# Kernel tuning notes

Measured on AMD Instinct MI355X. Metric: run time of the kernel, lower is better.

Reference implementation:

```python
import jax, jax.numpy as jnp
import numpy as np

N_NODES = 100000
N_EDGES = 1600000
NEG_SLOPE = 0.2  # PyG GATConv default


def _gat_layer(x, src, dst, W, a_src, a_dst, b, heads, concat):
    """One PyG-style GATConv (eval mode, self-loops already appended)."""
    N = x.shape[0]
    xp = (x @ W).reshape(N, heads, -1)                      # [N, H, C]
    al_s = jnp.einsum('nhc,hc->nh', xp, a_src)              # [N, H]
    al_d = jnp.einsum('nhc,hc->nh', xp, a_dst)              # [N, H]
    e = jax.nn.leaky_relu(al_s[src] + al_d[dst], NEG_SLOPE)  # [E, H]
    # numerically stable segment softmax over incoming edges of each dst
    m = jax.ops.segment_max(e, dst, num_segments=N)         # [N, H]
    ex = jnp.exp(e - m[dst])
    s = jax.ops.segment_sum(ex, dst, num_segments=N)
    alpha = ex / (s[dst] + 1e-16)                           # [E, H]
    out = jax.ops.segment_sum(xp[src] * alpha[:, :, None], dst, num_segments=N)  # [N, H, C]
    out = out.reshape(N, -1) if concat else out.mean(axis=1)
    return out + b


def setup_inputs() -> dict:
    key = jax.random.key(0)
    ks = jax.random.split(key, 16)
    H, C0 = 4, 32  # hidden layers: 4 heads x 32 = 128
    inp = {
        'x': jax.random.normal(ks[0], (N_NODES, 128), dtype=jnp.float32),
        'edge_index': jax.random.randint(ks[1], (2, N_EDGES), 0, N_NODES, dtype=jnp.int64),
        'W0': jax.random.normal(ks[2], (128, 128), dtype=jnp.float32) * 0.1,
        'a_src0': jax.random.normal(ks[3], (H, C0), dtype=jnp.float32) * 0.1,
        'a_dst0': jax.random.normal(ks[4], (H, C0), dtype=jnp.float32) * 0.1,
        'b0': jnp.zeros((128,), dtype=jnp.float32),
        'W1': jax.random.normal(ks[5], (128, 128), dtype=jnp.float32) * 0.1,
        'a_src1': jax.random.normal(ks[6], (H, C0), dtype=jnp.float32) * 0.1,
        'a_dst1': jax.random.normal(ks[7], (H, C0), dtype=jnp.float32) * 0.1,
        'b1': jnp.zeros((128,), dtype=jnp.float32),
        'W2': jax.random.normal(ks[8], (128, 64), dtype=jnp.float32) * 0.1,
        'a_src2': jax.random.normal(ks[9], (1, 64), dtype=jnp.float32) * 0.1,
        'a_dst2': jax.random.normal(ks[10], (1, 64), dtype=jnp.float32) * 0.1,
        'b2': jnp.zeros((64,), dtype=jnp.float32),
    }
    return inp


def reference(x, edge_index, W0, a_src0, a_dst0, b0, W1, a_src1, a_dst1, b1, W2, a_src2, a_dst2, b2):
    N = x.shape[0]
    loop = jnp.arange(N, dtype=edge_index.dtype)
    src = jnp.concatenate([edge_index[0], loop])  # add_self_loops=True
    dst = jnp.concatenate([edge_index[1], loop])
    h = _gat_layer(x, src, dst, W0, a_src0, a_dst0, b0, heads=4, concat=True)
    h = jax.nn.elu(h)
    h = _gat_layer(h, src, dst, W1, a_src1, a_dst1, b1, heads=4, concat=True)
    h = jax.nn.elu(h)
    out = _gat_layer(h, src, dst, W2, a_src2, a_dst2, b2, heads=1, concat=False)
    return out
```

## Files before the change

### kernel.cpp

```cpp
#include <hip/hip_runtime.h>
#include <math.h>


#define N_NODES 100000
#define NBUCK ((N_NODES + 255) / 256)

typedef __attribute__((ext_vector_type(4))) _Float16 half4;
typedef __attribute__((ext_vector_type(8))) _Float16 half8;
typedef __attribute__((ext_vector_type(4))) float f32x4;


__global__ __launch_bounds__(256) void k_bcount(const int* __restrict__ ei, int E, int ETOT,
                                                int* __restrict__ bucketCnt) {
    __shared__ int h[NBUCK];
    for (int b = threadIdx.x; b < NBUCK; b += 256) h[b] = 0;
    __syncthreads();
    const int base = blockIdx.x * 4096;
#pragma unroll
    for (int j = 0; j < 16; ++j) {
        int idx = base + j * 256 + threadIdx.x;
        if (idx < ETOT) {
            int dst = (idx < E) ? ei[E + idx] : (idx - E);
            atomicAdd(&h[dst >> 8], 1);
        }
    }
    __syncthreads();
    for (int b = threadIdx.x; b < NBUCK; b += 256)
        if (h[b]) atomicAdd(&bucketCnt[b], h[b]);
}

__global__ __launch_bounds__(256) void k_bscan(const int* __restrict__ bucketCnt,
                                               int* __restrict__ bstart,
                                               int* __restrict__ gcur, int ETOT) {
    __shared__ int lds[512];
    const int t = threadIdx.x;
    lds[t] = (t < NBUCK) ? bucketCnt[t] : 0;
    lds[t + 256] = (t + 256 < NBUCK) ? bucketCnt[t + 256] : 0;
    __syncthreads();
    for (int d = 1; d < 512; d <<= 1) {
        int v0 = (t >= d) ? lds[t - d] : 0;
        int v1 = (t + 256 >= d) ? lds[t + 256 - d] : 0;
        __syncthreads();
        lds[t] += v0;
        lds[t + 256] += v1;
        __syncthreads();
    }
    int e0 = (t == 0) ? 0 : lds[t - 1];
    int e1 = lds[t + 255];
    if (t < NBUCK)       { bstart[t] = e0;       gcur[t] = e0; }
    if (t + 256 < NBUCK) { bstart[t + 256] = e1; gcur[t + 256] = e1; }
    if (t == 0) bstart[NBUCK] = ETOT;
}

__global__ __launch_bounds__(256) void k_bplace(const int* __restrict__ ei, int E, int ETOT,
                                                int* __restrict__ gcur, int* __restrict__ tmp) {
    __shared__ int h[NBUCK];
    __shared__ int cur[NBUCK];
    for (int b = threadIdx.x; b < NBUCK; b += 256) h[b] = 0;
    __syncthreads();
    const int base = blockIdx.x * 4096;
    int pk[16], bk[16];
#pragma unroll
    for (int j = 0; j < 16; ++j) {
        int idx = base + j * 256 + threadIdx.x;
        bk[j] = -1;
        if (idx < ETOT) {
            int s, d;
            if (idx < E) { s = ei[idx]; d = ei[E + idx]; }
            else         { s = idx - E; d = idx - E; }
            bk[j] = d >> 8;
            pk[j] = s | ((d & 255) << 17);
            atomicAdd(&h[bk[j]], 1);
        }
    }
    __syncthreads();
    for (int b = threadIdx.x; b < NBUCK; b += 256)
        cur[b] = h[b] ? atomicAdd(&gcur[b], h[b]) : 0;
    __syncthreads();
#pragma unroll
    for (int j = 0; j < 16; ++j) {
        if (bk[j] >= 0) {
            int pos = atomicAdd(&cur[bk[j]], 1);
            tmp[pos] = pk[j];
        }
    }
}

__global__ __launch_bounds__(256) void k_bfinal(const int* __restrict__ tmp,
                                                const int* __restrict__ bstart,
                                                int* __restrict__ rowptr,
                                                int* __restrict__ ssrc, int N) {
    __shared__ int cnt[256];
    __shared__ int cur[256];
    const int t = threadIdx.x;
    const int b = blockIdx.x;
    const int s0 = bstart[b], s1 = bstart[b + 1];
    cnt[t] = 0;
    __syncthreads();
    for (int e = s0 + t; e < s1; e += 256)
        atomicAdd(&cnt[tmp[e] >> 17], 1);
    __syncthreads();
    int c0 = cnt[t];
    for (int d = 1; d < 256; d <<= 1) {
        int v = (t >= d) ? cnt[t - d] : 0;
        __syncthreads();
        cnt[t] += v;
        __syncthreads();
    }
    int excl = cnt[t] - c0;
    int node = b * 256 + t;
    if (node <= N) rowptr[node] = s0 + excl;
    cur[t] = excl;
    __syncthreads();
    for (int e = s0 + t; e < s1; e += 256) {
        int p = tmp[e];
        int pos = atomicAdd(&cur[p >> 17], 1);
        ssrc[s0 + pos] = p & 0x1FFFF;
    }
}

__global__ void k_wt(const float* __restrict__ W, _Float16* __restrict__ Wt, int OUTn) {
    int idx = blockIdx.x * 256 + threadIdx.x;
    if (idx >= 128 * OUTn) return;
    int k = idx / OUTn, n = idx % OUTn;
    Wt[n * 128 + k] = (_Float16)W[idx];
}

template <int OUT, int H>
__global__ __launch_bounds__(256) void k_gemm(const float* __restrict__ X,
                                              const _Float16* __restrict__ Wt,
                                              const float* __restrict__ a_src,
                                              const float* __restrict__ a_dst,
                                              _Float16* __restrict__ XP,
                                              float* __restrict__ al_s,
                                              float* __restrict__ al_d, int N) {
    constexpr int NT = OUT / 16;
    constexpr int C = OUT / H;
    constexpr int LDH = 136;
    __shared__ _Float16 As[64 * LDH];
    __shared__ _Float16 Ws[OUT * LDH];
    const int tid = threadIdx.x;
    const int row0 = blockIdx.x * 64;

    for (int c = tid; c < OUT * 16; c += 256) {
        int r = c >> 4, kc = c & 15;
        *(half8*)&Ws[r * LDH + kc * 8] = *(const half8*)(Wt + r * 128 + kc * 8);
    }
    for (int c = tid; c < 64 * 16; c += 256) {
        int r = c >> 4, kc = c & 15;
        int grow = row0 + r;
        half8 hv;
        if (grow < N) {
            const float4* xr = (const float4*)(X + (size_t)grow * 128 + kc * 8);
            float4 x0 = xr[0], x1 = xr[1];
            hv[0] = (_Float16)x0.x; hv[1] = (_Float16)x0.y;
            hv[2] = (_Float16)x0.z; hv[3] = (_Float16)x0.w;
            hv[4] = (_Float16)x1.x; hv[5] = (_Float16)x1.y;
            hv[6] = (_Float16)x1.z; hv[7] = (_Float16)x1.w;
        } else {
#pragma unroll
            for (int j = 0; j < 8; ++j) hv[j] = (_Float16)0.f;
        }
        *(half8*)&As[r * LDH + kc * 8] = hv;
    }
    __syncthreads();

    const int w = tid >> 6;
    const int l = tid & 63;
    const int lm = l & 15;
    const int lk = l >> 4;

    f32x4 acc[NT];
#pragma unroll
    for (int nt = 0; nt < NT; ++nt) acc[nt] = {0.f, 0.f, 0.f, 0.f};

#pragma unroll
    for (int ks = 0; ks < 4; ++ks) {
        half8 av = *(const half8*)&As[(w * 16 + lm) * LDH + ks * 32 + lk * 8];
#pragma unroll
        for (int nt = 0; nt < NT; ++nt) {
            half8 bv = *(const half8*)&Ws[(nt * 16 + lm) * LDH + ks * 32 + lk * 8];
            acc[nt] = __builtin_amdgcn_mfma_f32_16x16x32_f16(av, bv, acc[nt], 0, 0, 0);
        }
    }

    float avs[NT], avd[NT];
#pragma unroll
    for (int nt = 0; nt < NT; ++nt) {
        avs[nt] = a_src[nt * 16 + lm];
        avd[nt] = a_dst[nt * 16 + lm];
    }

#pragma unroll
    for (int r = 0; r < 4; ++r) {
        int grow = row0 + w * 16 + lk * 4 + r;
        bool ok = grow < N;
#pragma unroll
        for (int nt = 0; nt < NT; ++nt)
            if (ok) XP[(size_t)grow * OUT + nt * 16 + lm] = (_Float16)acc[nt][r];

        float ps[H], pd[H];
#pragma unroll
        for (int h = 0; h < H; ++h) { ps[h] = 0.f; pd[h] = 0.f; }
#pragma unroll
        for (int nt = 0; nt < NT; ++nt) {
            int h = (nt * 16) / C;
            ps[h] += acc[nt][r] * avs[nt];
            pd[h] += acc[nt][r] * avd[nt];
        }
#pragma unroll
        for (int h = 0; h < H; ++h) {
#pragma unroll
            for (int o = 8; o >= 1; o >>= 1) {
                ps[h] += __shfl_xor(ps[h], o);
                pd[h] += __shfl_xor(pd[h], o);
            }
        }
        if (ok && lm == 0) {
#pragma unroll
            for (int h = 0; h < H; ++h) {
                al_s[(size_t)grow * H + h] = ps[h];
                al_d[(size_t)grow * H + h] = pd[h];
            }
        }
    }
}

template <int OUT, int H, bool ELU>
__global__ __launch_bounds__(256) void k_agg(const _Float16* __restrict__ xp,
                                             const float* __restrict__ al_s,
                                             const float* __restrict__ al_d,
                                             const int* __restrict__ rowptr,
                                             const int* __restrict__ ssrc,
                                             const float* __restrict__ bias,
                                             float* __restrict__ out, int N) {
    constexpr int C = OUT / H;
    constexpr int CPL = OUT / 16;
    const int wid = threadIdx.x >> 6;
    const int lane = threadIdx.x & 63;
    const int qid = lane >> 4;
    const int l4 = lane & 15;
    const int node = blockIdx.x * 4 + wid;
    if (node >= N) return;
    const int rs = rowptr[node];
    const int re = rowptr[node + 1];

    const int c0 = l4 * CPL;
    const int hd = c0 / C;
    const float adh = al_d[(size_t)node * H + hd];

    float ssum = 0.f;
    float acc[CPL];
#pragma unroll
    for (int j = 0; j < CPL; ++j) acc[j] = 0.f;

    int i = rs;
    for (; i + 8 <= re; i += 8) {
        int sA = ssrc[i + qid];
        int sB = ssrc[i + qid + 4];
        float eA = al_s[(size_t)sA * H + hd] + adh; eA = eA > 0.f ? eA : 0.2f * eA;
        float eB = al_s[(size_t)sB * H + hd] + adh; eB = eB > 0.f ? eB : 0.2f * eB;
        float aA = __expf(eA);
        float aB = __expf(eB);
        ssum += aA + aB;
        if constexpr (CPL == 8) {
            half8 vA = *(const half8*)(xp + (size_t)sA * OUT + c0);
            half8 vB = *(const half8*)(xp + (size_t)sB * OUT + c0);
#pragma unroll
            for (int j = 0; j < 8; ++j) acc[j] += aA * (float)vA[j] + aB * (float)vB[j];
        } else {
            half4 vA = *(const half4*)(xp + (size_t)sA * OUT + c0);
            half4 vB = *(const half4*)(xp + (size_t)sB * OUT + c0);
#pragma unroll
            for (int j = 0; j < 4; ++j) acc[j] += aA * (float)vA[j] + aB * (float)vB[j];
        }
    }
    for (; i + qid < re; i += 4) {
        int s = ssrc[i + qid];
        float e = al_s[(size_t)s * H + hd] + adh; e = e > 0.f ? e : 0.2f * e;
        float a = __expf(e);
        ssum += a;
        if constexpr (CPL == 8) {
            half8 v = *(const half8*)(xp + (size_t)s * OUT + c0);
#pragma unroll
            for (int j = 0; j < 8; ++j) acc[j] += a * (float)v[j];
        } else {
            half4 v = *(const half4*)(xp + (size_t)s * OUT + c0);
#pragma unroll
            for (int j = 0; j < 4; ++j) acc[j] += a * (float)v[j];
        }
    }

    ssum += __shfl_xor(ssum, 16);
    ssum += __shfl_xor(ssum, 32);
#pragma unroll
    for (int j = 0; j < CPL; ++j) {
        acc[j] += __shfl_xor(acc[j], 16);
        acc[j] += __shfl_xor(acc[j], 32);
    }

    if (qid == 0) {
        float inv = 1.f / (ssum + 1e-16f);
        float o[CPL];
#pragma unroll
        for (int j = 0; j < CPL; ++j) {
            o[j] = acc[j] * inv + bias[c0 + j];
            if constexpr (ELU) o[j] = o[j] > 0.f ? o[j] : (__expf(o[j]) - 1.f);
        }
        float* op = out + (size_t)node * OUT + c0;
        if constexpr (CPL == 8) {
            *(float4*)op = make_float4(o[0], o[1], o[2], o[3]);
            *(float4*)(op + 4) = make_float4(o[4], o[5], o[6], o[7]);
        } else {
            *(float4*)op = make_float4(o[0], o[1], o[2], o[3]);
        }
    }
}


extern "C" void kernel_launch(void* const* d_in, const int* in_sizes, int n_in,
                              void* d_out, int out_size, void* d_ws, size_t ws_size,
                              hipStream_t stream) {
    const int N = N_NODES;
    const float* x     = (const float*)d_in[0];
    const int*   ei    = (const int*)d_in[1];
    const float* W0    = (const float*)d_in[2];
    const float* as0   = (const float*)d_in[3];
    const float* ad0   = (const float*)d_in[4];
    const float* b0    = (const float*)d_in[5];
    const float* W1    = (const float*)d_in[6];
    const float* as1   = (const float*)d_in[7];
    const float* ad1   = (const float*)d_in[8];
    const float* b1    = (const float*)d_in[9];
    const float* W2    = (const float*)d_in[10];
    const float* as2   = (const float*)d_in[11];
    const float* ad2   = (const float*)d_in[12];
    const float* b2    = (const float*)d_in[13];
    float* out = (float*)d_out;

    const int E = in_sizes[1] / 2;
    const int ETOT = E + N;

    char* p = (char*)d_ws;
    auto alloc = [&](size_t bytes) {
        void* r = (void*)p;
        p += (bytes + 255) & ~(size_t)255;
        return r;
    };
    _Float16* xp    = (_Float16*)alloc((size_t)N * 128 * 2);
    float* hbuf     = (float*)alloc((size_t)N * 128 * 4);
    float* als      = (float*)alloc((size_t)N * 4 * 4);
    float* ald      = (float*)alloc((size_t)N * 4 * 4);
    int*   rowptr   = (int*)alloc((size_t)(N + 1) * 4);
    int*   ssrc     = (int*)alloc((size_t)ETOT * 4);
    int*   tmp      = (int*)alloc((size_t)ETOT * 4);
    int*   bucketCnt= (int*)alloc((size_t)NBUCK * 4);
    int*   bstart   = (int*)alloc((size_t)(NBUCK + 1) * 4);
    int*   gcur     = (int*)alloc((size_t)NBUCK * 4);
    _Float16* wt0   = (_Float16*)alloc((size_t)128 * 128 * 2);
    _Float16* wt1   = (_Float16*)alloc((size_t)128 * 128 * 2);
    _Float16* wt2   = (_Float16*)alloc((size_t)128 * 64 * 2);

    k_wt<<<64, 256, 0, stream>>>(W0, wt0, 128);
    k_wt<<<64, 256, 0, stream>>>(W1, wt1, 128);
    k_wt<<<32, 256, 0, stream>>>(W2, wt2, 64);

    const int PB = (ETOT + 4095) / 4096;
    hipMemsetAsync(bucketCnt, 0, (size_t)NBUCK * 4, stream);
    k_bcount<<<PB, 256, 0, stream>>>(ei, E, ETOT, bucketCnt);
    k_bscan<<<1, 256, 0, stream>>>(bucketCnt, bstart, gcur, ETOT);
    k_bplace<<<PB, 256, 0, stream>>>(ei, E, ETOT, gcur, tmp);
    k_bfinal<<<NBUCK, 256, 0, stream>>>(tmp, bstart, rowptr, ssrc, N);

    const int gGemm = (N + 63) / 64;
    const int gAgg  = (N + 3) / 4;

    k_gemm<128, 4><<<gGemm, 256, 0, stream>>>(x, wt0, as0, ad0, xp, als, ald, N);
    k_agg<128, 4, true><<<gAgg, 256, 0, stream>>>(xp, als, ald, rowptr, ssrc, b0, hbuf, N);

    k_gemm<128, 4><<<gGemm, 256, 0, stream>>>(hbuf, wt1, as1, ad1, xp, als, ald, N);
    k_agg<128, 4, true><<<gAgg, 256, 0, stream>>>(xp, als, ald, rowptr, ssrc, b1, hbuf, N);

    k_gemm<64, 1><<<gGemm, 256, 0, stream>>>(hbuf, wt2, as2, ad2, xp, als, ald, N);
    k_agg<64, 1, false><<<gAgg, 256, 0, stream>>>(xp, als, ald, rowptr, ssrc, b2, out, N);
}
```

Measured before the change: 339.6 us.

## Store hidden activations in fp16, merge weight transposes, unroll aggregation by 16

Intermediate hidden activations between layers are now written by the aggregation kernel as fp16 and read directly by the next GEMM. This halves the write and read traffic for the N x 128 hidden buffer, at the cost of rounding post-ELU values to fp16 (the GEMM already converted them to fp16). The three weight-transpose launches are merged into one kernel, and the aggregation edge loop is unrolled to four edges per lane so more gathers are in flight.

New measurement: 322.0 us. -5.2%, faster.

```diff
diff --git a/kernel.cpp b/kernel.cpp
--- a/kernel.cpp
+++ b/kernel.cpp
@@ -119,15 +119,26 @@
     }
 }
 
-__global__ void k_wt(const float* __restrict__ W, _Float16* __restrict__ Wt, int OUTn) {
+__global__ void k_wt3(const float* __restrict__ W0, const float* __restrict__ W1,
+                      const float* __restrict__ W2, _Float16* __restrict__ wt0,
+                      _Float16* __restrict__ wt1, _Float16* __restrict__ wt2) {
     int idx = blockIdx.x * 256 + threadIdx.x;
-    if (idx >= 128 * OUTn) return;
-    int k = idx / OUTn, n = idx % OUTn;
-    Wt[n * 128 + k] = (_Float16)W[idx];
-}
-
-template <int OUT, int H>
-__global__ __launch_bounds__(256) void k_gemm(const float* __restrict__ X,
+    if (idx < 16384) {
+        int k = idx >> 7, n = idx & 127;
+        wt0[n * 128 + k] = (_Float16)W0[idx];
+    } else if (idx < 32768) {
+        int i = idx - 16384;
+        int k = i >> 7, n = i & 127;
+        wt1[n * 128 + k] = (_Float16)W1[i];
+    } else if (idx < 40960) {
+        int i = idx - 32768;
+        int k = i >> 6, n = i & 63;
+        wt2[n * 128 + k] = (_Float16)W2[i];
+    }
+}
+
+template <int OUT, int H, bool INF16>
+__global__ __launch_bounds__(256) void k_gemm(const void* __restrict__ Xv_,
                                               const _Float16* __restrict__ Wt,
                                               const float* __restrict__ a_src,
                                               const float* __restrict__ a_dst,
@@ -151,12 +162,16 @@
         int grow = row0 + r;
         half8 hv;
         if (grow < N) {
-            const float4* xr = (const float4*)(X + (size_t)grow * 128 + kc * 8);
-            float4 x0 = xr[0], x1 = xr[1];
-            hv[0] = (_Float16)x0.x; hv[1] = (_Float16)x0.y;
-            hv[2] = (_Float16)x0.z; hv[3] = (_Float16)x0.w;
-            hv[4] = (_Float16)x1.x; hv[5] = (_Float16)x1.y;
-            hv[6] = (_Float16)x1.z; hv[7] = (_Float16)x1.w;
+            if constexpr (INF16) {
+                hv = *(const half8*)((const _Float16*)Xv_ + (size_t)grow * 128 + kc * 8);
+            } else {
+                const float4* xr = (const float4*)((const float*)Xv_ + (size_t)grow * 128 + kc * 8);
+                float4 x0 = xr[0], x1 = xr[1];
+                hv[0] = (_Float16)x0.x; hv[1] = (_Float16)x0.y;
+                hv[2] = (_Float16)x0.z; hv[3] = (_Float16)x0.w;
+                hv[4] = (_Float16)x1.x; hv[5] = (_Float16)x1.y;
+                hv[6] = (_Float16)x1.z; hv[7] = (_Float16)x1.w;
+            }
         } else {
 #pragma unroll
             for (int j = 0; j < 8; ++j) hv[j] = (_Float16)0.f;
@@ -226,14 +241,14 @@
     }
 }
 
-template <int OUT, int H, bool ELU>
+template <int OUT, int H, bool ELU, bool OUTF16>
 __global__ __launch_bounds__(256) void k_agg(const _Float16* __restrict__ xp,
                                              const float* __restrict__ al_s,
                                              const float* __restrict__ al_d,
                                              const int* __restrict__ rowptr,
                                              const int* __restrict__ ssrc,
                                              const float* __restrict__ bias,
-                                             float* __restrict__ out, int N) {
+                                             void* __restrict__ out_, int N) {
     constexpr int C = OUT / H;
     constexpr int CPL = OUT / 16;
     const int wid = threadIdx.x >> 6;
@@ -254,30 +269,10 @@
 #pragma unroll
     for (int j = 0; j < CPL; ++j) acc[j] = 0.f;
 
-    int i = rs;
-    for (; i + 8 <= re; i += 8) {
-        int sA = ssrc[i + qid];
-        int sB = ssrc[i + qid + 4];
-        float eA = al_s[(size_t)sA * H + hd] + adh; eA = eA > 0.f ? eA : 0.2f * eA;
-        float eB = al_s[(size_t)sB * H + hd] + adh; eB = eB > 0.f ? eB : 0.2f * eB;
-        float aA = __expf(eA);
-        float aB = __expf(eB);
-        ssum += aA + aB;
-        if constexpr (CPL == 8) {
-            half8 vA = *(const half8*)(xp + (size_t)sA * OUT + c0);
-            half8 vB = *(const half8*)(xp + (size_t)sB * OUT + c0);
-#pragma unroll
-            for (int j = 0; j < 8; ++j) acc[j] += aA * (float)vA[j] + aB * (float)vB[j];
-        } else {
-            half4 vA = *(const half4*)(xp + (size_t)sA * OUT + c0);
-            half4 vB = *(const half4*)(xp + (size_t)sB * OUT + c0);
-#pragma unroll
-            for (int j = 0; j < 4; ++j) acc[j] += aA * (float)vA[j] + aB * (float)vB[j];
-        }
-    }
-    for (; i + qid < re; i += 4) {
-        int s = ssrc[i + qid];
-        float e = al_s[(size_t)s * H + hd] + adh; e = e > 0.f ? e : 0.2f * e;
+    auto edge = [&](int idx) {
+        int s = ssrc[idx];
+        float e = al_s[(size_t)s * H + hd] + adh;
+        e = e > 0.f ? e : 0.2f * e;
         float a = __expf(e);
         ssum += a;
         if constexpr (CPL == 8) {
@@ -289,6 +284,17 @@
 #pragma unroll
             for (int j = 0; j < 4; ++j) acc[j] += a * (float)v[j];
         }
+    };
+
+    int i = rs;
+    for (; i + 16 <= re; i += 16) {
+        edge(i + qid); edge(i + qid + 4); edge(i + qid + 8); edge(i + qid + 12);
+    }
+    for (; i + 8 <= re; i += 8) {
+        edge(i + qid); edge(i + qid + 4);
+    }
+    for (; i + qid < re; i += 4) {
+        edge(i + qid);
     }
 
     ssum += __shfl_xor(ssum, 16);
@@ -307,12 +313,27 @@
             o[j] = acc[j] * inv + bias[c0 + j];
             if constexpr (ELU) o[j] = o[j] > 0.f ? o[j] : (__expf(o[j]) - 1.f);
         }
-        float* op = out + (size_t)node * OUT + c0;
-        if constexpr (CPL == 8) {
-            *(float4*)op = make_float4(o[0], o[1], o[2], o[3]);
-            *(float4*)(op + 4) = make_float4(o[4], o[5], o[6], o[7]);
+        if constexpr (OUTF16) {
+            _Float16* op = (_Float16*)out_ + (size_t)node * OUT + c0;
+            if constexpr (CPL == 8) {
+                half8 hv;
+#pragma unroll
+                for (int j = 0; j < 8; ++j) hv[j] = (_Float16)o[j];
+                *(half8*)op = hv;
+            } else {
+                half4 hv;
+#pragma unroll
+                for (int j = 0; j < 4; ++j) hv[j] = (_Float16)o[j];
+                *(half4*)op = hv;
+            }
         } else {
-            *(float4*)op = make_float4(o[0], o[1], o[2], o[3]);
+            float* op = (float*)out_ + (size_t)node * OUT + c0;
+            if constexpr (CPL == 8) {
+                *(float4*)op = make_float4(o[0], o[1], o[2], o[3]);
+                *(float4*)(op + 4) = make_float4(o[4], o[5], o[6], o[7]);
+            } else {
+                *(float4*)op = make_float4(o[0], o[1], o[2], o[3]);
+            }
         }
     }
 }
@@ -348,7 +369,7 @@
         return r;
     };
     _Float16* xp    = (_Float16*)alloc((size_t)N * 128 * 2);
-    float* hbuf     = (float*)alloc((size_t)N * 128 * 4);
+    _Float16* hbuf  = (_Float16*)alloc((size_t)N * 128 * 2);
     float* als      = (float*)alloc((size_t)N * 4 * 4);
     float* ald      = (float*)alloc((size_t)N * 4 * 4);
     int*   rowptr   = (int*)alloc((size_t)(N + 1) * 4);
@@ -361,9 +382,7 @@
     _Float16* wt1   = (_Float16*)alloc((size_t)128 * 128 * 2);
     _Float16* wt2   = (_Float16*)alloc((size_t)128 * 64 * 2);
 
-    k_wt<<<64, 256, 0, stream>>>(W0, wt0, 128);
-    k_wt<<<64, 256, 0, stream>>>(W1, wt1, 128);
-    k_wt<<<32, 256, 0, stream>>>(W2, wt2, 64);
+    k_wt3<<<160, 256, 0, stream>>>(W0, W1, W2, wt0, wt1, wt2);
 
     const int PB = (ETOT + 4095) / 4096;
     hipMemsetAsync(bucketCnt, 0, (size_t)NBUCK * 4, stream);
@@ -375,12 +394,12 @@
     const int gGemm = (N + 63) / 64;
     const int gAgg  = (N + 3) / 4;
 
-    k_gemm<128, 4><<<gGemm, 256, 0, stream>>>(x, wt0, as0, ad0, xp, als, ald, N);
-    k_agg<128, 4, true><<<gAgg, 256, 0, stream>>>(xp, als, ald, rowptr, ssrc, b0, hbuf, N);
-
-    k_gemm<128, 4><<<gGemm, 256, 0, stream>>>(hbuf, wt1, as1, ad1, xp, als, ald, N);
-    k_agg<128, 4, true><<<gAgg, 256, 0, stream>>>(xp, als, ald, rowptr, ssrc, b1, hbuf, N);
-
-    k_gemm<64, 1><<<gGemm, 256, 0, stream>>>(hbuf, wt2, as2, ad2, xp, als, ald, N);
-    k_agg<64, 1, false><<<gAgg, 256, 0, stream>>>(xp, als, ald, rowptr, ssrc, b2, out, N);
-}
+    k_gemm<128, 4, false><<<gGemm, 256, 0, stream>>>(x, wt0, as0, ad0, xp, als, ald, N);
+    k_agg<128, 4, true, true><<<gAgg, 256, 0, stream>>>(xp, als, ald, rowptr, ssrc, b0, hbuf, N);
+
+    k_gemm<128, 4, true><<<gGemm, 256, 0, stream>>>(hbuf, wt1, as1, ad1, xp, als, ald, N);
+    k_agg<128, 4, true, true><<<gAgg, 256, 0, stream>>>(xp, als, ald, rowptr, ssrc, b1, hbuf, N);
+
+    k_gemm<64, 1, true><<<gGemm, 256, 0, stream>>>(hbuf, wt2, as2, ad2, xp, als, ald, N);
+    k_agg<64, 1, false, false><<<gAgg, 256, 0, stream>>>(xp, als, ald, rowptr, ssrc, b2, out, N);
+}
```
